# Performance work log

Measured on AMD Instinct MI355X. Metric: run time of the kernel, lower is better.

## Reference

```python
import jax, jax.numpy as jnp
import numpy as np

B, IN, OUT, LAT = 8192, 256, 256, 128

def setup_inputs() -> dict:
    key = jax.random.key(0)
    ks = jax.random.split(key, 6)
    s = 0.05
    return {
        "x": jax.random.normal(ks[0], (B, IN), dtype=jnp.float32),
        "latent": jax.random.normal(ks[1], (B, LAT), dtype=jnp.float32),
        "Ww": jax.random.normal(ks[2], (LAT, IN * OUT), dtype=jnp.float32) * s,
        "bw": jax.random.normal(ks[3], (IN * OUT,), dtype=jnp.float32) * s,
        "Wb": jax.random.normal(ks[4], (LAT, OUT), dtype=jnp.float32) * s,
        "bb": jax.random.normal(ks[5], (OUT,), dtype=jnp.float32) * s,
    }

def reference(x, latent, Ww, bw, Wb, bb):
    lead = x.shape[:-1]
    x2 = x.reshape(-1, x.shape[-1])            # [B, in]
    l2 = latent.reshape(-1, latent.shape[-1])  # [B, lat]
    # per-sample weight: [B, in, out]
    weight = (l2 @ Ww + bw).reshape(-1, IN, OUT)
    # per-sample bias: [B, out]
    bias = l2 @ Wb + bb
    out = jnp.einsum('bi,bio->bo', x2, weight) + bias
    return out.reshape(*lead, OUT)
```

## Files before the change

kernel.cpp:

```cpp
#include <hip/hip_runtime.h>
#include <cstdint>
#include <cstddef>

#define BATCH  8192
#define IN_N   256
#define OUT_N  256
#define LAT_N  128
#define SLABS  129
#define KT     (SLABS * IN_N)
#define KT16   (KT / 16)
#define SPLITK 4

typedef _Float16 h8 __attribute__((ext_vector_type(8)));
typedef _Float16 h4 __attribute__((ext_vector_type(4)));
typedef _Float16 h2 __attribute__((ext_vector_type(2)));
typedef float    f16v __attribute__((ext_vector_type(16)));
typedef float    f4v  __attribute__((ext_vector_type(4)));

#define AS1 __attribute__((address_space(1)))
#define AS3 __attribute__((address_space(3)))
#define WAITVM0 asm volatile("s_waitcnt vmcnt(0)" ::: "memory")
#define WAITVM2 asm volatile("s_waitcnt vmcnt(2)" ::: "memory")
#define WAITVM4 asm volatile("s_waitcnt vmcnt(4)" ::: "memory")

#define WS_BP    0
#define WS_XH    16908288
#define WS_LT    21102592
#define WS_PARTS 23216128

#define PR_T1   516
#define PR_L1   580
#define PR_X1   1604
#define PR_O1   1608
#define PR_B1   2632
__global__ void k_prep(const float* __restrict__ Ww, const float* __restrict__ bw,
                       const float* __restrict__ x,  const float* __restrict__ latent,
                       const float* __restrict__ Wb, const float* __restrict__ bb,
                       _Float16* __restrict__ Bp, _Float16* __restrict__ Xh,
                       _Float16* __restrict__ LT, float* __restrict__ part0) {
    __shared__ _Float16 smemh[16512];
    const int bid = blockIdx.x;
    const int t   = threadIdx.x;

    if (bid < PR_T1) {
        _Float16* tile = smemh;
        const int k0 = bid * 64;
#pragma unroll
        for (int j = 0; j < 16; ++j) {
            int idx = j * 256 + t;
            int row = idx >> 6, col = (idx & 63) * 4;
            int k = k0 + row;
            const float* src = (k < LAT_N * IN_N)
                             ? Ww + (size_t)k * 256 + col
                             : bw + (size_t)(k - LAT_N * IN_N) * 256 + col;
            float4 v = *(const float4*)src;
            h4 o;
            o[0] = (_Float16)v.x; o[1] = (_Float16)v.y;
            o[2] = (_Float16)v.z; o[3] = (_Float16)v.w;
            *(h4*)(tile + row * 256 + col) = o;
        }
        __syncthreads();
        const int tl = t & 31;
#pragma unroll
        for (int j = 0; j < 4; ++j) {
            int stid = j * 8 + (t >> 5);
            int kt_l = stid >> 3, nt = stid & 7;
            int kt16 = bid * 4 + kt_l;
            _Float16* dst = Bp + ((size_t)(nt * KT16 + kt16) * 64) * 8;
#pragma unroll
            for (int kh = 0; kh < 2; ++kh) {
                h8 v;
#pragma unroll
                for (int h = 0; h < 8; ++h)
                    v[h] = tile[(kt_l * 16 + kh * 8 + h) * 256 + nt * 32 + tl];
                *(h8*)(dst + (size_t)(kh * 32 + tl) * 8) = v;
            }
        }
    } else if (bid < PR_L1) {
        _Float16* t2 = smemh;
        const int b0 = (bid - PR_T1) * 128;
#pragma unroll
        for (int j = 0; j < 16; ++j) {
            int idx = j * 256 + t;
            int b = idx >> 5, l = (idx & 31) * 4;
            float4 v = *(const float4*)(latent + (size_t)(b0 + b) * 128 + l);
            t2[(l + 0) * 129 + b] = (_Float16)v.x;
            t2[(l + 1) * 129 + b] = (_Float16)v.y;
            t2[(l + 2) * 129 + b] = (_Float16)v.z;
            t2[(l + 3) * 129 + b] = (_Float16)v.w;
        }
        __syncthreads();
#pragma unroll
        for (int j = 0; j < 32; ++j) {
            int idx = j * 256 + t;
            int l = idx >> 6, bb2 = (idx & 63) * 2;
            h2 w;
            w[0] = t2[l * 129 + bb2];
            w[1] = t2[l * 129 + bb2 + 1];
            *(h2*)(LT + (size_t)l * BATCH + b0 + bb2) = w;
        }
    } else if (bid < PR_X1) {
        const int cb = bid - PR_L1;
        int i = (cb * 256 + t) * 8;
        float4 v0 = *(const float4*)(x + i);
        float4 v1 = *(const float4*)(x + i + 4);
        h8 o;
        o[0] = (_Float16)v0.x; o[1] = (_Float16)v0.y;
        o[2] = (_Float16)v0.z; o[3] = (_Float16)v0.w;
        o[4] = (_Float16)v1.x; o[5] = (_Float16)v1.y;
        o[6] = (_Float16)v1.z; o[7] = (_Float16)v1.w;
        *(h8*)(Xh + i) = o;
    } else if (bid < PR_O1) {
        const int ob = bid - PR_X1;
        int base = ob * 2048 + t * 8;
        h8 o;
#pragma unroll
        for (int h = 0; h < 8; ++h) o[h] = (_Float16)1.0f;
        *(h8*)(LT + (size_t)LAT_N * BATCH + base) = o;
    } else {
        float* lat = (float*)smemh;
        const int b0 = (bid - PR_O1) * 8;
#pragma unroll
        for (int j = 0; j < 4; ++j) {
            int idx = t + 256 * j;
            int rr = idx >> 7, l = idx & 127;
            lat[rr * 128 + l] = latent[(size_t)(b0 + rr) * 128 + l];
        }
        __syncthreads();
        const int o = t;
        float acc[8];
        float bbv = bb[o];
#pragma unroll
        for (int rr = 0; rr < 8; ++rr) acc[rr] = bbv;
        for (int l = 0; l < 128; ++l) {
            float w = Wb[l * 256 + o];
#pragma unroll
            for (int rr = 0; rr < 8; ++rr) acc[rr] += lat[rr * 128 + l] * w;
        }
#pragma unroll
        for (int rr = 0; rr < 8; ++rr) part0[(size_t)(b0 + rr) * 256 + o] = acc[rr];
    }
}

__global__ __launch_bounds__(256, 2) void k_gemm(const _Float16* __restrict__ Bp,
                                                 const _Float16* __restrict__ Xh,
                                                 const _Float16* __restrict__ LT,
                                                 float* __restrict__ parts) {
    __shared__ __align__(16) _Float16 Bs[4 * 4096];

    const int bid   = blockIdx.x;
    const int ks    = bid & 3;
    const int nb    = (bid >> 2) & 1;
    const int m_blk = bid >> 3;
    const int m0    = m_blk * 128;
    const int slab0 = (ks == 0) ? 0 : 33 + 32 * (ks - 1);
    const int nslab = (ks == 0) ? 33 : 32;

    const int tid = threadIdx.x, wid = tid >> 6, lane = tid & 63;
    const int l32 = lane & 31, khalf = lane >> 5;
    const int wm = wid >> 1, wn = wid & 1;
    const int mrow0 = m0 + wm * 64 + l32;
    const int mrow1 = mrow0 + 32;

    h8 xv0[16], xv1[16];
    const _Float16* xp0 = Xh + (size_t)mrow0 * IN_N + khalf * 8;
    const _Float16* xp1 = Xh + (size_t)mrow1 * IN_N + khalf * 8;
#pragma unroll
    for (int k = 0; k < 16; ++k) {
        xv0[k] = *(const h8*)(xp0 + k * 16);
        xv1[k] = *(const h8*)(xp1 + k * 16);
    }

    const _Float16* ltp = LT + (size_t)slab0 * BATCH;
    _Float16 sc0 = ltp[mrow0], sc1 = ltp[mrow1];

    const int chunk0 = wid * 2;
    const char* Bgb = (const char*)Bp;

#define STAGE(bufidx, ktg)                                                                 \
    _Pragma("unroll")                                                                      \
    for (int i_ = 0; i_ < 2; ++i_) {                                                       \
        const int c_   = chunk0 + i_;                                                      \
        const int ktl_ = c_ >> 2, ntl_ = c_ & 3;                                           \
        const int ntg_ = nb * 4 + ntl_;                                                    \
        const char* g_ = Bgb + (((size_t)(ntg_ * KT16 + (ktg) + ktl_)) << 10) + (lane << 4);\
        _Float16* l_ = Bs + (bufidx) * 4096 + c_ * 512;                                    \
        __builtin_amdgcn_global_load_lds((const AS1 void*)g_, (AS3 void*)l_, 16, 0, 0);    \
    }

    f16v acc00, acc01, acc10, acc11;
#pragma unroll
    for (int r = 0; r < 16; ++r) { acc00[r] = 0.f; acc01[r] = 0.f; acc10[r] = 0.f; acc11[r] = 0.f; }

#define KSTEP(bufc, sl)                                                                    \
    _Pragma("unroll")                                                                      \
    for (int j = 0; j < 2; ++j) {                                                          \
        const int kx = (((sl) * 2 + j) & 15);                                              \
        h8 a0 = xv0[kx] * s80;                                                             \
        h8 a1 = xv1[kx] * s81;                                                             \
        const _Float16* bb = Bs + (bufc) * 4096 + j * 2048 + wn * 1024 + (lane << 3);      \
        h8 b0 = *(const h8*)(bb);                                                          \
        h8 b1 = *(const h8*)(bb + 512);                                                    \
        __builtin_amdgcn_s_setprio(1);                                                     \
        acc00 = __builtin_amdgcn_mfma_f32_32x32x16_f16(a0, b0, acc00, 0, 0, 0);            \
        acc01 = __builtin_amdgcn_mfma_f32_32x32x16_f16(a0, b1, acc01, 0, 0, 0);            \
        acc10 = __builtin_amdgcn_mfma_f32_32x32x16_f16(a1, b0, acc10, 0, 0, 0);            \
        acc11 = __builtin_amdgcn_mfma_f32_32x32x16_f16(a1, b1, acc11, 0, 0, 0);            \
        __builtin_amdgcn_s_setprio(0);                                                     \
    }

    const int kb = slab0 * 16;

    STAGE(0, kb + 0);
    STAGE(1, kb + 2);
    WAITVM2;
    __builtin_amdgcn_s_barrier();
    asm volatile("" ::: "memory");

    for (int s0 = 0; s0 < nslab - 1; ++s0) {
        _Float16 sn0 = ltp[(size_t)(s0 + 1) * BATCH + mrow0];
        _Float16 sn1 = ltp[(size_t)(s0 + 1) * BATCH + mrow1];
        h8 s80, s81;
#pragma unroll
        for (int h = 0; h < 8; ++h) { s80[h] = sc0; s81[h] = sc1; }
        const int ktg0 = kb + s0 * 16;
#pragma unroll
        for (int sl = 0; sl < 8; ++sl) {
            STAGE((sl + 2) & 3, ktg0 + (sl + 2) * 2);
            KSTEP(sl & 3, sl);
            if (sl == 0) WAITVM4; else WAITVM2;
            __builtin_amdgcn_s_barrier();
            asm volatile("" ::: "memory");
        }
        sc0 = sn0; sc1 = sn1;
    }

    {
        h8 s80, s81;
#pragma unroll
        for (int h = 0; h < 8; ++h) { s80[h] = sc0; s81[h] = sc1; }
        const int ktg0 = kb + (nslab - 1) * 16;
#pragma unroll
        for (int sl = 0; sl < 8; ++sl) {
            if (sl < 6) STAGE((sl + 2) & 3, ktg0 + (sl + 2) * 2);
            KSTEP(sl & 3, sl);
            if (sl < 7) {
                if (sl == 6) WAITVM0; else WAITVM2;
                __builtin_amdgcn_s_barrier();
                asm volatile("" ::: "memory");
            }
        }
    }

    float* dst = parts + (size_t)ks * ((size_t)BATCH * OUT_N);
    const int rowb0 = m0 + wm * 64;
#define EPI(rowb, u, accv)                                                                 \
    {                                                                                      \
        int col = nb * 128 + wn * 64 + (u) * 32 + l32;                                     \
        _Pragma("unroll")                                                                  \
        for (int r = 0; r < 16; ++r) {                                                     \
            int row = (rowb) + (r & 3) + 8 * (r >> 2) + 4 * khalf;                         \
            size_t off = (size_t)row * OUT_N + col;                                        \
            if (ks == 0) dst[off] += accv[r];                                              \
            else         dst[off] = accv[r];                                               \
        }                                                                                  \
    }
    EPI(rowb0,      0, acc00); EPI(rowb0,      1, acc01);
    EPI(rowb0 + 32, 0, acc10); EPI(rowb0 + 32, 1, acc11);
#undef EPI
#undef KSTEP
#undef STAGE
}

__global__ void k_reduce(const float* __restrict__ parts, float* __restrict__ out) {
    int i = (blockIdx.x * 256 + threadIdx.x) * 4;
    f4v s = *(const f4v*)(parts + i);
    s += *(const f4v*)(parts + 2097152 + i);
    s += *(const f4v*)(parts + 2 * 2097152 + i);
    s += *(const f4v*)(parts + 3 * 2097152 + i);
    *(f4v*)(out + i) = s;
}

extern "C" void kernel_launch(void* const* d_in, const int* in_sizes, int n_in,
                              void* d_out, int out_size, void* d_ws, size_t ws_size,
                              hipStream_t stream) {
    const float* x      = (const float*)d_in[0];
    const float* latent = (const float*)d_in[1];
    const float* Ww     = (const float*)d_in[2];
    const float* bw     = (const float*)d_in[3];
    const float* Wb     = (const float*)d_in[4];
    const float* bb     = (const float*)d_in[5];

    char* ws = (char*)d_ws;
    _Float16* Bp    = (_Float16*)(ws + WS_BP);
    _Float16* Xh    = (_Float16*)(ws + WS_XH);
    _Float16* LT    = (_Float16*)(ws + WS_LT);
    float*    parts = (float*)(ws + WS_PARTS);
    float*    out   = (float*)d_out;

    k_prep<<<PR_B1, 256, 0, stream>>>(Ww, bw, x, latent, Wb, bb, Bp, Xh, LT, parts);
    k_gemm<<<512, 256, 0, stream>>>(Bp, Xh, LT, parts);
    k_reduce<<<2048, 256, 0, stream>>>(parts, out);
}
```

Before: 253.4 us.

## Deepen LDS prefetch to three stages and double-buffer B fragments in registers

```diff
diff --git a/kernel.cpp b/kernel.cpp
--- a/kernel.cpp
+++ b/kernel.cpp
@@ -142,7 +142,7 @@
     }
 }
 
-__global__ __launch_bounds__(256, 2) void k_gemm(const _Float16* __restrict__ Bp,
+__global__ __launch_bounds__(256, 1) void k_gemm(const _Float16* __restrict__ Bp,
                                                  const _Float16* __restrict__ Xh,
                                                  const _Float16* __restrict__ LT,
                                                  float* __restrict__ parts) {
@@ -188,34 +188,50 @@
         __builtin_amdgcn_global_load_lds((const AS1 void*)g_, (AS3 void*)l_, 16, 0, 0);    \
     }
 
+#define DSREAD(d0, d1, d2, d3, bufc)                                                       \
+    {                                                                                      \
+        const _Float16* bb_ = Bs + (bufc) * 4096 + wn * 1024 + (lane << 3);                \
+        d0 = *(const h8*)(bb_);                                                            \
+        d1 = *(const h8*)(bb_ + 512);                                                      \
+        d2 = *(const h8*)(bb_ + 2048);                                                     \
+        d3 = *(const h8*)(bb_ + 2560);                                                     \
+    }
+
     f16v acc00, acc01, acc10, acc11;
 #pragma unroll
     for (int r = 0; r < 16; ++r) { acc00[r] = 0.f; acc01[r] = 0.f; acc10[r] = 0.f; acc11[r] = 0.f; }
 
-#define KSTEP(bufc, sl)                                                                    \
-    _Pragma("unroll")                                                                      \
-    for (int j = 0; j < 2; ++j) {                                                          \
-        const int kx = (((sl) * 2 + j) & 15);                                              \
-        h8 a0 = xv0[kx] * s80;                                                             \
-        h8 a1 = xv1[kx] * s81;                                                             \
-        const _Float16* bb = Bs + (bufc) * 4096 + j * 2048 + wn * 1024 + (lane << 3);      \
-        h8 b0 = *(const h8*)(bb);                                                          \
-        h8 b1 = *(const h8*)(bb + 512);                                                    \
+#define KSTEPR(sl)                                                                         \
+    {                                                                                      \
+        const int kx0 = (((sl) * 2 + 0) & 15), kx1 = (((sl) * 2 + 1) & 15);                \
+        h8 a00 = xv0[kx0] * s80;                                                           \
+        h8 a10 = xv1[kx0] * s81;                                                           \
         __builtin_amdgcn_s_setprio(1);                                                     \
-        acc00 = __builtin_amdgcn_mfma_f32_32x32x16_f16(a0, b0, acc00, 0, 0, 0);            \
-        acc01 = __builtin_amdgcn_mfma_f32_32x32x16_f16(a0, b1, acc01, 0, 0, 0);            \
-        acc10 = __builtin_amdgcn_mfma_f32_32x32x16_f16(a1, b0, acc10, 0, 0, 0);            \
-        acc11 = __builtin_amdgcn_mfma_f32_32x32x16_f16(a1, b1, acc11, 0, 0, 0);            \
+        acc00 = __builtin_amdgcn_mfma_f32_32x32x16_f16(a00, c0, acc00, 0, 0, 0);           \
+        acc01 = __builtin_amdgcn_mfma_f32_32x32x16_f16(a00, c1, acc01, 0, 0, 0);           \
+        acc10 = __builtin_amdgcn_mfma_f32_32x32x16_f16(a10, c0, acc10, 0, 0, 0);           \
+        acc11 = __builtin_amdgcn_mfma_f32_32x32x16_f16(a10, c1, acc11, 0, 0, 0);           \
         __builtin_amdgcn_s_setprio(0);                                                     \
+        h8 a01 = xv0[kx1] * s80;                                                           \
+        h8 a11 = xv1[kx1] * s81;                                                           \
+        __builtin_amdgcn_s_setprio(1);                                                     \
+        acc00 = __builtin_amdgcn_mfma_f32_32x32x16_f16(a01, c2, acc00, 0, 0, 0);           \
+        acc01 = __builtin_amdgcn_mfma_f32_32x32x16_f16(a01, c3, acc01, 0, 0, 0);           \
+        acc10 = __builtin_amdgcn_mfma_f32_32x32x16_f16(a11, c2, acc10, 0, 0, 0);           \
+        acc11 = __builtin_amdgcn_mfma_f32_32x32x16_f16(a11, c3, acc11, 0, 0, 0);           \
+        __builtin_amdgcn_s_setprio(0);                                                     \
     }
 
     const int kb = slab0 * 16;
+    h8 c0, c1, c2, c3, n0, n1, n2, n3;
 
     STAGE(0, kb + 0);
     STAGE(1, kb + 2);
+    STAGE(2, kb + 4);
     WAITVM2;
     __builtin_amdgcn_s_barrier();
     asm volatile("" ::: "memory");
+    DSREAD(c0, c1, c2, c3, 0);
 
     for (int s0 = 0; s0 < nslab - 1; ++s0) {
         _Float16 sn0 = ltp[(size_t)(s0 + 1) * BATCH + mrow0];
@@ -226,11 +242,13 @@
         const int ktg0 = kb + s0 * 16;
 #pragma unroll
         for (int sl = 0; sl < 8; ++sl) {
-            STAGE((sl + 2) & 3, ktg0 + (sl + 2) * 2);
-            KSTEP(sl & 3, sl);
+            STAGE((sl + 3) & 3, ktg0 + (sl + 3) * 2);
+            DSREAD(n0, n1, n2, n3, (sl + 1) & 3);
+            KSTEPR(sl);
             if (sl == 0) WAITVM4; else WAITVM2;
             __builtin_amdgcn_s_barrier();
             asm volatile("" ::: "memory");
+            c0 = n0; c1 = n1; c2 = n2; c3 = n3;
         }
         sc0 = sn0; sc1 = sn1;
     }
@@ -242,13 +260,16 @@
         const int ktg0 = kb + (nslab - 1) * 16;
 #pragma unroll
         for (int sl = 0; sl < 8; ++sl) {
-            if (sl < 6) STAGE((sl + 2) & 3, ktg0 + (sl + 2) * 2);
-            KSTEP(sl & 3, sl);
-            if (sl < 7) {
-                if (sl == 6) WAITVM0; else WAITVM2;
+            if (sl <= 4) STAGE((sl + 3) & 3, ktg0 + (sl + 3) * 2);
+            if (sl < 7) DSREAD(n0, n1, n2, n3, (sl + 1) & 3);
+            KSTEPR(sl);
+            if (sl <= 4) WAITVM2;
+            else if (sl == 5) WAITVM0;
+            if (sl <= 5) {
                 __builtin_amdgcn_s_barrier();
                 asm volatile("" ::: "memory");
             }
+            if (sl < 7) { c0 = n0; c1 = n1; c2 = n2; c3 = n3; }
         }
     }
 
@@ -268,7 +289,8 @@
     EPI(rowb0,      0, acc00); EPI(rowb0,      1, acc01);
     EPI(rowb0 + 32, 0, acc10); EPI(rowb0 + 32, 1, acc11);
 #undef EPI
-#undef KSTEP
+#undef KSTEPR
+#undef DSREAD
 #undef STAGE
 }
 
```

After: 282.1 us. +11.4%, slower.
